# Performance work log

Hardware: AMD Instinct MI355X
Metric: run time of the kernel (lower is better)

## Reference

```python
import jax, jax.numpy as jnp
import numpy as np

B, S, D, H = 2, 2048, 1024, 16
DK = D // H
NEG = -65504.0  # matches torch masked_fill value in source


def setup_inputs() -> dict:
    key = jax.random.key(0)
    ks = jax.random.split(key, 5)
    scale = 1.0 / np.sqrt(D)
    return {
        "x": jax.random.normal(ks[0], (B, S, D), dtype=jnp.float32),
        "W_q": jax.random.normal(ks[1], (D, D), dtype=jnp.float32) * scale,
        "W_k": jax.random.normal(ks[2], (D, D), dtype=jnp.float32) * scale,
        "W_v": jax.random.normal(ks[3], (D, D), dtype=jnp.float32) * scale,
        "W_o": jax.random.normal(ks[4], (D, D), dtype=jnp.float32) * scale,
    }


def reference(x, W_q, W_k, W_v, W_o):
    b, s, d = x.shape
    # nn.Linear(x) = x @ W.T ; split heads -> [b, h, s, dk]
    def proj(W):
        return (x @ W.T).reshape(b, s, H, DK).transpose(0, 2, 1, 3)
    q, k, v = proj(W_q), proj(W_k), proj(W_v)
    scores = jnp.einsum("bhqd,bhkd->bhqk", q, k) / jnp.sqrt(jnp.float32(DK))
    causal = jnp.tril(jnp.ones((s, s), dtype=bool))  # True where attending allowed
    scores = jnp.where(causal, scores, NEG)
    attn = jax.nn.softmax(scores, axis=-1)  # attn_pdrop=0 -> dropout is identity
    out = jnp.einsum("bhqk,bhkd->bhqd", attn, v)
    out = out.transpose(0, 2, 1, 3).reshape(b, s, d)
    return out @ W_o.T
```

## Files before the change

kernel.cpp:

```cpp
#include <hip/hip_runtime.h>
#include <hip/hip_bf16.h>

typedef __attribute__((ext_vector_type(4))) float f32x4;
typedef __attribute__((ext_vector_type(8))) short bf16x8;

#define Bn 2
#define Sn 2048
#define Dn 1024
#define Hn 16
#define DKn 64
#define Mrows (Bn * Sn)

__device__ __forceinline__ unsigned short f2bf(float f) {
  unsigned int x = __float_as_uint(f);
  x += 0x7fffu + ((x >> 16) & 1u);
  return (unsigned short)(x >> 16);
}

__device__ __forceinline__ float bf2f(unsigned short u) {
  return __uint_as_float(((unsigned int)u) << 16);
}

__device__ __forceinline__ unsigned int cvtpk(float lo, float hi) {
  unsigned int r;
  asm("v_cvt_pk_bf16_f32 %0, %1, %2" : "=v"(r) : "v"(lo), "v"(hi));
  return r;
}

__device__ __forceinline__ float exp2a(float x) {
  float r;
  asm("v_exp_f32 %0, %1" : "=v"(r) : "v"(x));
  return r;
}

__device__ __forceinline__ f32x4 mfma16(bf16x8 a, bf16x8 b, f32x4 c) {
  return __builtin_amdgcn_mfma_f32_16x16x32_bf16(a, b, c, 0, 0, 0);
}

__device__ __forceinline__ f32x4 max4(f32x4 a, f32x4 b) {
  f32x4 r;
  r[0] = fmaxf(a[0], b[0]); r[1] = fmaxf(a[1], b[1]);
  r[2] = fmaxf(a[2], b[2]); r[3] = fmaxf(a[3], b[3]);
  return r;
}

__device__ __forceinline__ void gload_lds16(const unsigned short* g, unsigned short* l) {
  __builtin_amdgcn_global_load_lds(
      (const __attribute__((address_space(1))) void*)g,
      (__attribute__((address_space(3))) void*)l, 16, 0, 0);
}

__global__ __launch_bounds__(256)
void cvt_all(const float* __restrict__ x,  const float* __restrict__ wq,
             const float* __restrict__ wk, const float* __restrict__ wv,
             const float* __restrict__ wo,
             unsigned short* __restrict__ xb,  unsigned short* __restrict__ wqb,
             unsigned short* __restrict__ wkb, unsigned short* __restrict__ wvb,
             unsigned short* __restrict__ wob) {
  int i = (blockIdx.x * 256 + threadIdx.x) * 4;
  const float* src; unsigned short* dst; int off;
  int r = i >> 20;
  if (r < 4)       { src = x;  dst = xb;  off = i; }
  else if (r == 4) { src = wq; dst = wqb; off = i & 1048575; }
  else if (r == 5) { src = wk; dst = wkb; off = i & 1048575; }
  else if (r == 6) { src = wv; dst = wvb; off = i & 1048575; }
  else             { src = wo; dst = wob; off = i & 1048575; }
  float4 v = *(const float4*)(src + off);
  ushort4 o;
  o.x = f2bf(v.x); o.y = f2bf(v.y); o.z = f2bf(v.z); o.w = f2bf(v.w);
  *(ushort4*)(dst + off) = o;
}

template<int MODE>
__device__ __forceinline__ void gemm_body(const unsigned short* __restrict__ A,
                                          const unsigned short* __restrict__ W,
                                          unsigned short* __restrict__ Cb,
                                          float* __restrict__ Cf,
                                          unsigned short* As,
                                          unsigned short* Bs,
                                          int row0, int col0) {
  const int K = Dn, N = Dn;
  const int tid  = threadIdx.x;
  const int wid  = tid >> 6;
  const int lane = tid & 63;
  const int l15  = lane & 15;
  const int lg   = lane >> 4;
  const int wr = (wid >> 1) * 64;
  const int wc = (wid & 1) * 64;

  f32x4 acc[4][4] = {};

  const int lrow2 = lane >> 2;
  const int gs    = (lane & 3) ^ ((lane >> 3) & 3);
  const int swzr  = (l15 >> 1) & 3;

  auto stage = [&](int kt, int b) {
#pragma unroll
    for (int q = 0; q < 2; ++q) {
      int chunk = wid * 2 + q;
      int r = chunk * 16 + lrow2;
      gload_lds16(A + (size_t)(row0 + r) * K + kt + gs * 8,
                  &As[b * 4096 + chunk * 512]);
    }
#pragma unroll
    for (int q = 0; q < 2; ++q) {
      int chunk = wid * 2 + q;
      int r = chunk * 16 + lrow2;
      gload_lds16(W + (size_t)(col0 + r) * K + kt + gs * 8,
                  &Bs[b * 4096 + chunk * 512]);
    }
  };

  auto compute = [&](int b) {
    bf16x8 af[4], bfr[4];
#pragma unroll
    for (int m = 0; m < 4; ++m)
      af[m] = *(const bf16x8*)(&As[b * 4096 + (wr + m * 16 + l15) * 32 +
                                   ((lg ^ swzr) * 8)]);
#pragma unroll
    for (int n = 0; n < 4; ++n)
      bfr[n] = *(const bf16x8*)(&Bs[b * 4096 + (wc + n * 16 + l15) * 32 +
                                    ((lg ^ swzr) * 8)]);
    __builtin_amdgcn_s_setprio(1);
#pragma unroll
    for (int m = 0; m < 4; ++m)
#pragma unroll
      for (int n = 0; n < 4; ++n)
        acc[m][n] = mfma16(af[m], bfr[n], acc[m][n]);
    __builtin_amdgcn_s_setprio(0);
  };

  stage(0, 0);
  stage(32, 1);
  int cb = 0;
#pragma unroll 1
  for (int t = 0; t < 32; ++t) {
    if (t < 31) asm volatile("s_waitcnt vmcnt(4)" ::: "memory");
    else        asm volatile("s_waitcnt vmcnt(0)" ::: "memory");
    __builtin_amdgcn_sched_barrier(0);
    __builtin_amdgcn_s_barrier();
    __builtin_amdgcn_sched_barrier(0);
    if (t <= 29) {
      int sb = cb + 2; if (sb >= 3) sb -= 3;
      stage((t + 2) * 32, sb);
    }
    compute(cb);
    ++cb; if (cb == 3) cb = 0;
  }

#pragma unroll
  for (int m = 0; m < 4; ++m)
#pragma unroll
    for (int n = 0; n < 4; ++n) {
      int r0 = row0 + wr + m * 16 + lg * 4;
      int c  = col0 + wc + n * 16 + l15;
      if (MODE == 2) {
        int b = r0 >> 11, s = r0 & 2047;
        int h = c >> 6,  d = c & 63;
        ushort4 pw;
        pw.x = f2bf(acc[m][n][0]); pw.y = f2bf(acc[m][n][1]);
        pw.z = f2bf(acc[m][n][2]); pw.w = f2bf(acc[m][n][3]);
        *(ushort4*)(Cb + ((((size_t)b * Hn + h) * DKn + d) << 11) + s) = pw;
      } else {
#pragma unroll
        for (int j = 0; j < 4; ++j) {
          size_t idx = (size_t)(r0 + j) * N + c;
          float v = acc[m][n][j];
          if (MODE == 3)      Cf[idx] = v;
          else if (MODE == 0) Cb[idx] = f2bf(v * 0.18033688f);
          else                Cb[idx] = f2bf(v);
        }
      }
    }
}

__global__ __launch_bounds__(256, 3)
void gemm_qkv(const unsigned short* __restrict__ A,
              const unsigned short* __restrict__ W0,
              const unsigned short* __restrict__ W1,
              const unsigned short* __restrict__ W2,
              unsigned short* __restrict__ C0,
              unsigned short* __restrict__ C1,
              unsigned short* __restrict__ C2) {
  __shared__ unsigned short As[3 * 128 * 32];
  __shared__ unsigned short Bs[3 * 128 * 32];
  const int fid = blockIdx.x;
  const int panel = fid % 24;
  const int row0 = (fid / 24) * 128;
  const int col0 = (panel & 7) * 128;
  const int z = panel >> 3;
  if (z == 0)      gemm_body<0>(A, W0, C0, nullptr, As, Bs, row0, col0);
  else if (z == 1) gemm_body<1>(A, W1, C1, nullptr, As, Bs, row0, col0);
  else             gemm_body<2>(A, W2, C2, nullptr, As, Bs, row0, col0);
}

__global__ __launch_bounds__(256, 3)
void gemm_out(const unsigned short* __restrict__ A,
              const unsigned short* __restrict__ W,
              float* __restrict__ C) {
  __shared__ unsigned short As[3 * 128 * 32];
  __shared__ unsigned short Bs[3 * 128 * 32];
  gemm_body<3>(A, W, nullptr, C, As, Bs, blockIdx.x * 128, blockIdx.y * 128);
}

__global__ __launch_bounds__(256, 3)
void attn_part(const unsigned short* __restrict__ Qg,
               const unsigned short* __restrict__ Kg,
               const unsigned short* __restrict__ Vtg,
               unsigned short* __restrict__ Og,
               unsigned short* __restrict__ Pb,
               float* __restrict__ Pml) {
  const int bid = blockIdx.x;
  const int bh = bid & 31;
  const int j  = bid >> 5;
  const int bb = bh >> 4, hh = bh & 15;
  const int tid = threadIdx.x, wid = tid >> 6, lane = tid & 63;
  const int l15 = lane & 15, lg = lane >> 4;
  const int wq = wid * 32;
  const size_t baseQ = (size_t)bb * Sn * Dn + (size_t)hh * DKn;
  const size_t baseV = (size_t)bh * DKn * Sn;

  __shared__ unsigned short Ks[2][64 * 64];
  __shared__ unsigned short Vts[2][64 * 64];
  __shared__ unsigned short Ps[4][32 * 72];

  const int lrow  = lane >> 3;
  const int sgran = (lane & 7) ^ lrow;
  const int swz   = l15 & 7;

  const int bstart = (34 * j) / 3;
  const int nt = (34 * (j + 1)) / 3 - bstart;

  int qt = 0;
  while ((qt + 1) * (qt + 2) <= bstart) ++qt;
  int kt = bstart - qt * (qt + 1);

  int sqt = qt, skt = kt;
  auto stage = [&](int t, int b) {
    const int k0 = t << 6;
#pragma unroll
    for (int p = 0; p < 2; ++p) {
      int c = p * 4 + wid;
      int r = c * 8 + lrow;
      gload_lds16(Kg + baseQ + (size_t)(k0 + r) * Dn + sgran * 8, &Ks[b][c * 512]);
    }
#pragma unroll
    for (int p = 0; p < 2; ++p) {
      int c = p * 4 + wid;
      int dr = c * 8 + lrow;
      gload_lds16(Vtg + baseV + (size_t)dr * Sn + k0 + sgran * 8, &Vts[b][c * 512]);
    }
  };
  auto advs = [&]() { ++skt; if (skt == 2 * sqt + 2) { skt = 0; ++sqt; } };

  stage(skt, 0); advs();
  __syncthreads();

  bf16x8 qf[2][2];
  auto loadQ = [&](int qtile) {
    const int q0 = qtile * 128;
#pragma unroll
    for (int qm = 0; qm < 2; ++qm)
#pragma unroll
      for (int kd = 0; kd < 2; ++kd)
        qf[qm][kd] = *(const bf16x8*)(Qg + baseQ +
                     (size_t)(q0 + wq + qm * 16 + l15) * Dn + kd * 32 + lg * 8);
  };
  loadQ(qt);

  f32x4 oacc[2][4] = {};
  float mrun[2] = {-1e30f, -1e30f};
  float lrun[2] = {0.f, 0.f};
  int pstart = kt;

  for (int i = 0; i < nt; ++i) {
    const int cur = i & 1;
    if (i < nt - 1) { stage(skt, cur ^ 1); advs(); }
    const int k0 = kt << 6;
    const int q0 = qt * 128;

    if (k0 <= q0 + wq + 31) {
      f32x4 sf[2][4] = {};
      __builtin_amdgcn_s_setprio(1);
#pragma unroll
      for (int kn = 0; kn < 4; ++kn)
#pragma unroll
        for (int kd = 0; kd < 2; ++kd) {
          bf16x8 kf = *(const bf16x8*)(&Ks[cur][(kn * 16 + l15) * 64 +
                                              (((kd * 4 + lg) ^ swz) * 8)]);
          sf[0][kn] = mfma16(kf, qf[0][kd], sf[0][kn]);
          sf[1][kn] = mfma16(kf, qf[1][kd], sf[1][kn]);
        }
      __builtin_amdgcn_s_setprio(0);

      if (k0 + 63 > q0 + wq) {
#pragma unroll
        for (int qm = 0; qm < 2; ++qm) {
          int qq = q0 + wq + qm * 16 + l15;
#pragma unroll
          for (int kn = 0; kn < 4; ++kn)
#pragma unroll
            for (int jj = 0; jj < 4; ++jj) {
              int key = k0 + kn * 16 + lg * 4 + jj;
              if (key > qq) sf[qm][kn][jj] = -1e30f;
            }
        }
      }

#pragma unroll
      for (int qm = 0; qm < 2; ++qm) {
        f32x4 mm = max4(max4(sf[qm][0], sf[qm][1]), max4(sf[qm][2], sf[qm][3]));
        float tl = fmaxf(fmaxf(mm[0], mm[1]), fmaxf(mm[2], mm[3]));
        if (__any(tl > mrun[qm] + 11.5f)) {
          float t = tl;
          t = fmaxf(t, __shfl_xor(t, 16));
          t = fmaxf(t, __shfl_xor(t, 32));
          float mnew = fmaxf(mrun[qm], t);
          float corr = exp2a(mrun[qm] - mnew);
          mrun[qm] = mnew;
          lrun[qm] *= corr;
#pragma unroll
          for (int dn = 0; dn < 4; ++dn) oacc[qm][dn] *= corr;
        }
        const float m = mrun[qm];
#pragma unroll
        for (int kn = 0; kn < 4; ++kn) {
#pragma unroll
          for (int jj = 0; jj < 4; ++jj)
            sf[qm][kn][jj] = exp2a(sf[qm][kn][jj] - m);
          uint2 pw;
          pw.x = cvtpk(sf[qm][kn][0], sf[qm][kn][1]);
          pw.y = cvtpk(sf[qm][kn][2], sf[qm][kn][3]);
          *(uint2*)(&Ps[wid][(qm * 16 + l15) * 72 + kn * 16 + lg * 4]) = pw;
        }
        f32x4 sv = (sf[qm][0] + sf[qm][1]) + (sf[qm][2] + sf[qm][3]);
        lrun[qm] += (sv[0] + sv[1]) + (sv[2] + sv[3]);
      }

      __builtin_amdgcn_s_setprio(1);
#pragma unroll
      for (int kk = 0; kk < 2; ++kk) {
        bf16x8 pf[2];
#pragma unroll
        for (int qm = 0; qm < 2; ++qm)
          pf[qm] = *(const bf16x8*)(&Ps[wid][(qm * 16 + l15) * 72 + kk * 32 + lg * 8]);
#pragma unroll
        for (int dn = 0; dn < 4; ++dn) {
          bf16x8 vf = *(const bf16x8*)(&Vts[cur][(dn * 16 + l15) * 64 +
                                               (((kk * 4 + lg) ^ swz) * 8)]);
#pragma unroll
          for (int qm = 0; qm < 2; ++qm)
            oacc[qm][dn] = mfma16(vf, pf[qm], oacc[qm][dn]);
        }
      }
      __builtin_amdgcn_s_setprio(0);
    }

    const bool segend = (kt == 2 * qt + 1);
    if (segend || i == nt - 1) {
      if (pstart == 0 && segend) {
#pragma unroll
        for (int qm = 0; qm < 2; ++qm) {
          float lt = lrun[qm];
          lt += __shfl_xor(lt, 16);
          lt += __shfl_xor(lt, 32);
          float rinv = 1.0f / lt;
          int row = q0 + wq + qm * 16 + l15;
#pragma unroll
          for (int dn = 0; dn < 4; ++dn) {
            ushort4 ow;
            ow.x = f2bf(oacc[qm][dn][0] * rinv);
            ow.y = f2bf(oacc[qm][dn][1] * rinv);
            ow.z = f2bf(oacc[qm][dn][2] * rinv);
            ow.w = f2bf(oacc[qm][dn][3] * rinv);
            *(ushort4*)(Og + baseQ + (size_t)row * Dn + dn * 16 + lg * 4) = ow;
          }
        }
      } else {
        const size_t slot = (size_t)bh * 40 + (pstart == 0 ? qt : 16 + j);
#pragma unroll
        for (int qm = 0; qm < 2; ++qm) {
          float lt = lrun[qm];
          lt += __shfl_xor(lt, 16);
          lt += __shfl_xor(lt, 32);
          int rl = wq + qm * 16 + l15;
#pragma unroll
          for (int dn = 0; dn < 4; ++dn) {
            ushort4 ow;
            ow.x = f2bf(oacc[qm][dn][0]);
            ow.y = f2bf(oacc[qm][dn][1]);
            ow.z = f2bf(oacc[qm][dn][2]);
            ow.w = f2bf(oacc[qm][dn][3]);
            *(ushort4*)(Pb + slot * 8192 + (size_t)rl * 64 + dn * 16 + lg * 4) = ow;
          }
          if (lg == 0) {
            Pml[slot * 256 + rl] = mrun[qm];
            Pml[slot * 256 + 128 + rl] = lt;
          }
        }
      }
      if (i < nt - 1) {
        ++qt; kt = 0; pstart = 0;
        loadQ(qt);
#pragma unroll
        for (int qm = 0; qm < 2; ++qm) {
          mrun[qm] = -1e30f; lrun[qm] = 0.f;
#pragma unroll
          for (int dn = 0; dn < 4; ++dn) oacc[qm][dn] = f32x4{0.f, 0.f, 0.f, 0.f};
        }
      }
    } else {
      ++kt;
    }
    __syncthreads();
  }
}

__global__ __launch_bounds__(256)
void attn_combine(const unsigned short* __restrict__ Pb,
                  const float* __restrict__ Pml,
                  unsigned short* __restrict__ Og) {
  const int b = blockIdx.x;
  const int bh = b >> 4, qt = b & 15;
  const int s = qt * (qt + 1);
  const int e = s + 2 * qt + 2;
  const int js = (3 * s + 2) / 34;
  const int je = (3 * (e - 1) + 2) / 34;
  const int np = je - js + 1;
  if (np == 1) return;
  const int bb = bh >> 4, hh = bh & 15;
  const size_t baseQ = (size_t)bb * Sn * Dn + (size_t)hh * DKn;
  const int q0 = qt * 128;
  const int r = threadIdx.x >> 1;
  const int c32 = (threadIdx.x & 1) * 32;

  float M = -1e30f;
  for (int p = 0; p < np; ++p) {
    size_t slot = (size_t)bh * 40 + (p == 0 ? qt : 16 + js + p);
    M = fmaxf(M, Pml[slot * 256 + r]);
  }

  float L = 0.f;
  float acc[32];
#pragma unroll
  for (int k = 0; k < 32; ++k) acc[k] = 0.f;
  for (int p = 0; p < np; ++p) {
    size_t slot = (size_t)bh * 40 + (p == 0 ? qt : 16 + js + p);
    float w = exp2a(Pml[slot * 256 + r] - M);
    L += Pml[slot * 256 + 128 + r] * w;
    const unsigned short* src = Pb + slot * 8192 + (size_t)r * 64 + c32;
#pragma unroll
    for (int k4 = 0; k4 < 8; ++k4) {
      ushort4 v = *(const ushort4*)(src + k4 * 4);
      acc[k4 * 4 + 0] += w * bf2f(v.x);
      acc[k4 * 4 + 1] += w * bf2f(v.y);
      acc[k4 * 4 + 2] += w * bf2f(v.z);
      acc[k4 * 4 + 3] += w * bf2f(v.w);
    }
  }

  float rinv = 1.0f / L;
#pragma unroll
  for (int k4 = 0; k4 < 8; ++k4) {
    ushort4 o;
    o.x = f2bf(acc[k4 * 4 + 0] * rinv);
    o.y = f2bf(acc[k4 * 4 + 1] * rinv);
    o.z = f2bf(acc[k4 * 4 + 2] * rinv);
    o.w = f2bf(acc[k4 * 4 + 3] * rinv);
    *(ushort4*)(Og + baseQ + (size_t)(q0 + r) * Dn + c32 + k4 * 4) = o;
  }
}

extern "C" void kernel_launch(void* const* d_in, const int* in_sizes, int n_in,
                              void* d_out, int out_size, void* d_ws, size_t ws_size,
                              hipStream_t stream) {
  const float* x  = (const float*)d_in[0];
  const float* Wq = (const float*)d_in[1];
  const float* Wk = (const float*)d_in[2];
  const float* Wv = (const float*)d_in[3];
  const float* Wo = (const float*)d_in[4];
  float* out = (float*)d_out;

  char* ws = (char*)d_ws;
  size_t off = 0;
  unsigned short* xb  = (unsigned short*)(ws + off); off += (size_t)Mrows * Dn * 2;
  unsigned short* wqb = (unsigned short*)(ws + off); off += (size_t)Dn * Dn * 2;
  unsigned short* wkb = (unsigned short*)(ws + off); off += (size_t)Dn * Dn * 2;
  unsigned short* wvb = (unsigned short*)(ws + off); off += (size_t)Dn * Dn * 2;
  unsigned short* wob = (unsigned short*)(ws + off); off += (size_t)Dn * Dn * 2;
  unsigned short* Qb  = (unsigned short*)(ws + off); off += (size_t)Mrows * Dn * 2;
  unsigned short* Kb  = (unsigned short*)(ws + off); off += (size_t)Mrows * Dn * 2;
  unsigned short* Vtb = (unsigned short*)(ws + off); off += (size_t)Mrows * Dn * 2;
  unsigned short* Ob  = (unsigned short*)(ws + off); off += (size_t)Mrows * Dn * 2;
  unsigned short* Pb  = (unsigned short*)(ws + off); off += (size_t)1280 * 8192 * 2;
  float*          Pml = (float*)(ws + off);          off += (size_t)1280 * 256 * 4;

  cvt_all<<<8192, 256, 0, stream>>>(x, Wq, Wk, Wv, Wo, xb, wqb, wkb, wvb, wob);
  gemm_qkv<<<768, 256, 0, stream>>>(xb, wqb, wkb, wvb, Qb, Kb, Vtb);
  attn_part<<<768, 256, 0, stream>>>(Qb, Kb, Vtb, Ob, Pb, Pml);
  attn_combine<<<512, 256, 0, stream>>>(Pb, Pml, Ob);
  gemm_out<<<dim3(Mrows / 128, Dn / 128), 256, 0, stream>>>(Ob, wob, out);
}
```

Measured before the change: 110.2 us.

## Use 8-wave attention blocks with 16-row warps and uniform 17-tile work split

The attention partial kernel now runs 512 threads (8 waves), each wave owning 16 query rows instead of 32, which halves per-wave register state and allows more resident waves. Work is split evenly into 512 blocks of exactly 17 key tiles each, and partial-result slots are re-indexed per query tile (up to 3 per tile), with the combine kernel rewritten to use this fixed layout. This aims to improve latency hiding and load balance, at the cost of less reuse of each K/V fragment across query rows and more LDS reads per MFMA.

```diff
diff --git a/kernel.cpp b/kernel.cpp
--- a/kernel.cpp
+++ b/kernel.cpp
@@ -203,7 +203,7 @@
   gemm_body<3>(A, W, nullptr, C, As, Bs, blockIdx.x * 128, blockIdx.y * 128);
 }
 
-__global__ __launch_bounds__(256, 3)
+__global__ __launch_bounds__(512, 4)
 void attn_part(const unsigned short* __restrict__ Qg,
                const unsigned short* __restrict__ Kg,
                const unsigned short* __restrict__ Vtg,
@@ -216,71 +216,59 @@
   const int bb = bh >> 4, hh = bh & 15;
   const int tid = threadIdx.x, wid = tid >> 6, lane = tid & 63;
   const int l15 = lane & 15, lg = lane >> 4;
-  const int wq = wid * 32;
+  const int wq = wid * 16;
   const size_t baseQ = (size_t)bb * Sn * Dn + (size_t)hh * DKn;
   const size_t baseV = (size_t)bh * DKn * Sn;
 
   __shared__ unsigned short Ks[2][64 * 64];
   __shared__ unsigned short Vts[2][64 * 64];
-  __shared__ unsigned short Ps[4][32 * 72];
+  __shared__ unsigned short Ps[8][16 * 72];
 
   const int lrow  = lane >> 3;
   const int sgran = (lane & 7) ^ lrow;
   const int swz   = l15 & 7;
 
-  const int bstart = (34 * j) / 3;
-  const int nt = (34 * (j + 1)) / 3 - bstart;
-
+  const int g0 = 17 * j;
   int qt = 0;
-  while ((qt + 1) * (qt + 2) <= bstart) ++qt;
-  int kt = bstart - qt * (qt + 1);
+  while ((qt + 1) * (qt + 2) <= g0) ++qt;
+  int kt = g0 - qt * (qt + 1);
 
   int sqt = qt, skt = kt;
   auto stage = [&](int t, int b) {
     const int k0 = t << 6;
-#pragma unroll
-    for (int p = 0; p < 2; ++p) {
-      int c = p * 4 + wid;
-      int r = c * 8 + lrow;
-      gload_lds16(Kg + baseQ + (size_t)(k0 + r) * Dn + sgran * 8, &Ks[b][c * 512]);
-    }
-#pragma unroll
-    for (int p = 0; p < 2; ++p) {
-      int c = p * 4 + wid;
-      int dr = c * 8 + lrow;
-      gload_lds16(Vtg + baseV + (size_t)dr * Sn + k0 + sgran * 8, &Vts[b][c * 512]);
-    }
+    gload_lds16(Kg + baseQ + (size_t)(k0 + wid * 8 + lrow) * Dn + sgran * 8,
+                &Ks[b][wid * 512]);
+    gload_lds16(Vtg + baseV + (size_t)(wid * 8 + lrow) * Sn + k0 + sgran * 8,
+                &Vts[b][wid * 512]);
   };
   auto advs = [&]() { ++skt; if (skt == 2 * sqt + 2) { skt = 0; ++sqt; } };
 
   stage(skt, 0); advs();
   __syncthreads();
 
-  bf16x8 qf[2][2];
+  bf16x8 qf[2];
   auto loadQ = [&](int qtile) {
     const int q0 = qtile * 128;
 #pragma unroll
-    for (int qm = 0; qm < 2; ++qm)
-#pragma unroll
-      for (int kd = 0; kd < 2; ++kd)
-        qf[qm][kd] = *(const bf16x8*)(Qg + baseQ +
-                     (size_t)(q0 + wq + qm * 16 + l15) * Dn + kd * 32 + lg * 8);
+    for (int kd = 0; kd < 2; ++kd)
+      qf[kd] = *(const bf16x8*)(Qg + baseQ +
+               (size_t)(q0 + wq + l15) * Dn + kd * 32 + lg * 8);
   };
   loadQ(qt);
 
-  f32x4 oacc[2][4] = {};
-  float mrun[2] = {-1e30f, -1e30f};
-  float lrun[2] = {0.f, 0.f};
+  f32x4 oacc[4] = {};
+  float mrun = -1e30f;
+  float lrun = 0.f;
   int pstart = kt;
 
-  for (int i = 0; i < nt; ++i) {
+  for (int i = 0; i < 17; ++i) {
     const int cur = i & 1;
-    if (i < nt - 1) { stage(skt, cur ^ 1); advs(); }
+    if (i < 16) { stage(skt, cur ^ 1); advs(); }
     const int k0 = kt << 6;
     const int q0 = qt * 128;
 
-    if (k0 <= q0 + wq + 31) {
-      f32x4 sf[2][4] = {};
+    if (k0 <= q0 + wq + 15) {
+      f32x4 sf[4] = {};
       __builtin_amdgcn_s_setprio(1);
 #pragma unroll
       for (int kn = 0; kn < 4; ++kn)
@@ -288,126 +276,107 @@
         for (int kd = 0; kd < 2; ++kd) {
           bf16x8 kf = *(const bf16x8*)(&Ks[cur][(kn * 16 + l15) * 64 +
                                               (((kd * 4 + lg) ^ swz) * 8)]);
-          sf[0][kn] = mfma16(kf, qf[0][kd], sf[0][kn]);
-          sf[1][kn] = mfma16(kf, qf[1][kd], sf[1][kn]);
+          sf[kn] = mfma16(kf, qf[kd], sf[kn]);
         }
       __builtin_amdgcn_s_setprio(0);
 
       if (k0 + 63 > q0 + wq) {
-#pragma unroll
-        for (int qm = 0; qm < 2; ++qm) {
-          int qq = q0 + wq + qm * 16 + l15;
-#pragma unroll
-          for (int kn = 0; kn < 4; ++kn)
-#pragma unroll
-            for (int jj = 0; jj < 4; ++jj) {
-              int key = k0 + kn * 16 + lg * 4 + jj;
-              if (key > qq) sf[qm][kn][jj] = -1e30f;
-            }
-        }
-      }
-
-#pragma unroll
-      for (int qm = 0; qm < 2; ++qm) {
-        f32x4 mm = max4(max4(sf[qm][0], sf[qm][1]), max4(sf[qm][2], sf[qm][3]));
-        float tl = fmaxf(fmaxf(mm[0], mm[1]), fmaxf(mm[2], mm[3]));
-        if (__any(tl > mrun[qm] + 11.5f)) {
-          float t = tl;
-          t = fmaxf(t, __shfl_xor(t, 16));
-          t = fmaxf(t, __shfl_xor(t, 32));
-          float mnew = fmaxf(mrun[qm], t);
-          float corr = exp2a(mrun[qm] - mnew);
-          mrun[qm] = mnew;
-          lrun[qm] *= corr;
-#pragma unroll
-          for (int dn = 0; dn < 4; ++dn) oacc[qm][dn] *= corr;
-        }
-        const float m = mrun[qm];
-#pragma unroll
-        for (int kn = 0; kn < 4; ++kn) {
-#pragma unroll
-          for (int jj = 0; jj < 4; ++jj)
-            sf[qm][kn][jj] = exp2a(sf[qm][kn][jj] - m);
-          uint2 pw;
-          pw.x = cvtpk(sf[qm][kn][0], sf[qm][kn][1]);
-          pw.y = cvtpk(sf[qm][kn][2], sf[qm][kn][3]);
-          *(uint2*)(&Ps[wid][(qm * 16 + l15) * 72 + kn * 16 + lg * 4]) = pw;
-        }
-        f32x4 sv = (sf[qm][0] + sf[qm][1]) + (sf[qm][2] + sf[qm][3]);
-        lrun[qm] += (sv[0] + sv[1]) + (sv[2] + sv[3]);
-      }
+        int qq = q0 + wq + l15;
+#pragma unroll
+        for (int kn = 0; kn < 4; ++kn)
+#pragma unroll
+          for (int jj = 0; jj < 4; ++jj) {
+            int key = k0 + kn * 16 + lg * 4 + jj;
+            if (key > qq) sf[kn][jj] = -1e30f;
+          }
+      }
+
+      f32x4 mm = max4(max4(sf[0], sf[1]), max4(sf[2], sf[3]));
+      float tl = fmaxf(fmaxf(mm[0], mm[1]), fmaxf(mm[2], mm[3]));
+      if (__any(tl > mrun + 11.5f)) {
+        float t = tl;
+        t = fmaxf(t, __shfl_xor(t, 16));
+        t = fmaxf(t, __shfl_xor(t, 32));
+        float mnew = fmaxf(mrun, t);
+        float corr = exp2a(mrun - mnew);
+        mrun = mnew;
+        lrun *= corr;
+#pragma unroll
+        for (int dn = 0; dn < 4; ++dn) oacc[dn] *= corr;
+      }
+      const float m = mrun;
+#pragma unroll
+      for (int kn = 0; kn < 4; ++kn) {
+#pragma unroll
+        for (int jj = 0; jj < 4; ++jj)
+          sf[kn][jj] = exp2a(sf[kn][jj] - m);
+        uint2 pw;
+        pw.x = cvtpk(sf[kn][0], sf[kn][1]);
+        pw.y = cvtpk(sf[kn][2], sf[kn][3]);
+        *(uint2*)(&Ps[wid][l15 * 72 + kn * 16 + lg * 4]) = pw;
+      }
+      f32x4 sv = (sf[0] + sf[1]) + (sf[2] + sf[3]);
+      lrun += (sv[0] + sv[1]) + (sv[2] + sv[3]);
 
       __builtin_amdgcn_s_setprio(1);
 #pragma unroll
       for (int kk = 0; kk < 2; ++kk) {
-        bf16x8 pf[2];
-#pragma unroll
-        for (int qm = 0; qm < 2; ++qm)
-          pf[qm] = *(const bf16x8*)(&Ps[wid][(qm * 16 + l15) * 72 + kk * 32 + lg * 8]);
+        bf16x8 pf = *(const bf16x8*)(&Ps[wid][l15 * 72 + kk * 32 + lg * 8]);
 #pragma unroll
         for (int dn = 0; dn < 4; ++dn) {
           bf16x8 vf = *(const bf16x8*)(&Vts[cur][(dn * 16 + l15) * 64 +
                                                (((kk * 4 + lg) ^ swz) * 8)]);
-#pragma unroll
-          for (int qm = 0; qm < 2; ++qm)
-            oacc[qm][dn] = mfma16(vf, pf[qm], oacc[qm][dn]);
+          oacc[dn] = mfma16(vf, pf, oacc[dn]);
         }
       }
       __builtin_amdgcn_s_setprio(0);
     }
 
     const bool segend = (kt == 2 * qt + 1);
-    if (segend || i == nt - 1) {
+    if (segend || i == 16) {
       if (pstart == 0 && segend) {
-#pragma unroll
-        for (int qm = 0; qm < 2; ++qm) {
-          float lt = lrun[qm];
-          lt += __shfl_xor(lt, 16);
-          lt += __shfl_xor(lt, 32);
-          float rinv = 1.0f / lt;
-          int row = q0 + wq + qm * 16 + l15;
-#pragma unroll
-          for (int dn = 0; dn < 4; ++dn) {
-            ushort4 ow;
-            ow.x = f2bf(oacc[qm][dn][0] * rinv);
-            ow.y = f2bf(oacc[qm][dn][1] * rinv);
-            ow.z = f2bf(oacc[qm][dn][2] * rinv);
-            ow.w = f2bf(oacc[qm][dn][3] * rinv);
-            *(ushort4*)(Og + baseQ + (size_t)row * Dn + dn * 16 + lg * 4) = ow;
-          }
+        float lt = lrun;
+        lt += __shfl_xor(lt, 16);
+        lt += __shfl_xor(lt, 32);
+        float rinv = 1.0f / lt;
+        int row = q0 + wq + l15;
+#pragma unroll
+        for (int dn = 0; dn < 4; ++dn) {
+          ushort4 ow;
+          ow.x = f2bf(oacc[dn][0] * rinv);
+          ow.y = f2bf(oacc[dn][1] * rinv);
+          ow.z = f2bf(oacc[dn][2] * rinv);
+          ow.w = f2bf(oacc[dn][3] * rinv);
+          *(ushort4*)(Og + baseQ + (size_t)row * Dn + dn * 16 + lg * 4) = ow;
         }
       } else {
-        const size_t slot = (size_t)bh * 40 + (pstart == 0 ? qt : 16 + j);
-#pragma unroll
-        for (int qm = 0; qm < 2; ++qm) {
-          float lt = lrun[qm];
-          lt += __shfl_xor(lt, 16);
-          lt += __shfl_xor(lt, 32);
-          int rl = wq + qm * 16 + l15;
-#pragma unroll
-          for (int dn = 0; dn < 4; ++dn) {
-            ushort4 ow;
-            ow.x = f2bf(oacc[qm][dn][0]);
-            ow.y = f2bf(oacc[qm][dn][1]);
-            ow.z = f2bf(oacc[qm][dn][2]);
-            ow.w = f2bf(oacc[qm][dn][3]);
-            *(ushort4*)(Pb + slot * 8192 + (size_t)rl * 64 + dn * 16 + lg * 4) = ow;
-          }
-          if (lg == 0) {
-            Pml[slot * 256 + rl] = mrun[qm];
-            Pml[slot * 256 + 128 + rl] = lt;
-          }
-        }
-      }
-      if (i < nt - 1) {
+        const int seg_s = qt * (qt + 1);
+        const int ord = pstart ? ((seg_s + pstart) / 17 - seg_s / 17) : 0;
+        const size_t slot = (size_t)((bh * 16 + qt) * 3 + ord);
+        float lt = lrun;
+        lt += __shfl_xor(lt, 16);
+        lt += __shfl_xor(lt, 32);
+        int rl = wq + l15;
+#pragma unroll
+        for (int dn = 0; dn < 4; ++dn) {
+          ushort4 ow;
+          ow.x = f2bf(oacc[dn][0]);
+          ow.y = f2bf(oacc[dn][1]);
+          ow.z = f2bf(oacc[dn][2]);
+          ow.w = f2bf(oacc[dn][3]);
+          *(ushort4*)(Pb + slot * 8192 + (size_t)rl * 64 + dn * 16 + lg * 4) = ow;
+        }
+        if (lg == 0) {
+          Pml[slot * 256 + rl] = mrun;
+          Pml[slot * 256 + 128 + rl] = lt;
+        }
+      }
+      if (i < 16) {
         ++qt; kt = 0; pstart = 0;
         loadQ(qt);
-#pragma unroll
-        for (int qm = 0; qm < 2; ++qm) {
-          mrun[qm] = -1e30f; lrun[qm] = 0.f;
-#pragma unroll
-          for (int dn = 0; dn < 4; ++dn) oacc[qm][dn] = f32x4{0.f, 0.f, 0.f, 0.f};
-        }
+        mrun = -1e30f; lrun = 0.f;
+#pragma unroll
+        for (int dn = 0; dn < 4; ++dn) oacc[dn] = f32x4{0.f, 0.f, 0.f, 0.f};
       }
     } else {
       ++kt;
@@ -422,33 +391,38 @@
                   unsigned short* __restrict__ Og) {
   const int b = blockIdx.x;
   const int bh = b >> 4, qt = b & 15;
-  const int s = qt * (qt + 1);
-  const int e = s + 2 * qt + 2;
-  const int js = (3 * s + 2) / 34;
-  const int je = (3 * (e - 1) + 2) / 34;
-  const int np = je - js + 1;
-  if (np == 1) return;
+  const int seg_s = qt * (qt + 1);
+  const int seg_e = seg_s + 2 * qt + 2;
+  const int c0 = (seg_s / 17 + 1) * 17;
+  if (c0 >= seg_e) return;
+  const int np = (c0 + 17 < seg_e) ? 3 : 2;
   const int bb = bh >> 4, hh = bh & 15;
   const size_t baseQ = (size_t)bb * Sn * Dn + (size_t)hh * DKn;
   const int q0 = qt * 128;
+  const int slot0 = b * 3;
   const int r = threadIdx.x >> 1;
   const int c32 = (threadIdx.x & 1) * 32;
 
-  float M = -1e30f;
-  for (int p = 0; p < np; ++p) {
-    size_t slot = (size_t)bh * 40 + (p == 0 ? qt : 16 + js + p);
-    M = fmaxf(M, Pml[slot * 256 + r]);
+  float m0 = Pml[(size_t)slot0 * 256 + r];
+  float l0 = Pml[(size_t)slot0 * 256 + 128 + r];
+  float m1 = Pml[(size_t)(slot0 + 1) * 256 + r];
+  float l1 = Pml[(size_t)(slot0 + 1) * 256 + 128 + r];
+  float m2 = -1e30f, l2 = 0.f;
+  if (np == 3) {
+    m2 = Pml[(size_t)(slot0 + 2) * 256 + r];
+    l2 = Pml[(size_t)(slot0 + 2) * 256 + 128 + r];
   }
-
-  float L = 0.f;
+  float M = fmaxf(fmaxf(m0, m1), m2);
+  float w0 = exp2a(m0 - M), w1 = exp2a(m1 - M);
+  float w2 = (np == 3) ? exp2a(m2 - M) : 0.f;
+  float L = l0 * w0 + l1 * w1 + l2 * w2;
+
   float acc[32];
 #pragma unroll
   for (int k = 0; k < 32; ++k) acc[k] = 0.f;
-  for (int p = 0; p < np; ++p) {
-    size_t slot = (size_t)bh * 40 + (p == 0 ? qt : 16 + js + p);
-    float w = exp2a(Pml[slot * 256 + r] - M);
-    L += Pml[slot * 256 + 128 + r] * w;
-    const unsigned short* src = Pb + slot * 8192 + (size_t)r * 64 + c32;
+
+  auto accum = [&](int p, float w) {
+    const unsigned short* src = Pb + (size_t)(slot0 + p) * 8192 + (size_t)r * 64 + c32;
 #pragma unroll
     for (int k4 = 0; k4 < 8; ++k4) {
       ushort4 v = *(const ushort4*)(src + k4 * 4);
@@ -457,7 +431,10 @@
       acc[k4 * 4 + 2] += w * bf2f(v.z);
       acc[k4 * 4 + 3] += w * bf2f(v.w);
     }
-  }
+  };
+  accum(0, w0);
+  accum(1, w1);
+  if (np == 3) accum(2, w2);
 
   float rinv = 1.0f / L;
 #pragma unroll
@@ -492,12 +469,12 @@
   unsigned short* Kb  = (unsigned short*)(ws + off); off += (size_t)Mrows * Dn * 2;
   unsigned short* Vtb = (unsigned short*)(ws + off); off += (size_t)Mrows * Dn * 2;
   unsigned short* Ob  = (unsigned short*)(ws + off); off += (size_t)Mrows * Dn * 2;
-  unsigned short* Pb  = (unsigned short*)(ws + off); off += (size_t)1280 * 8192 * 2;
-  float*          Pml = (float*)(ws + off);          off += (size_t)1280 * 256 * 4;
+  unsigned short* Pb  = (unsigned short*)(ws + off); off += (size_t)1536 * 8192 * 2;
+  float*          Pml = (float*)(ws + off);          off += (size_t)1536 * 256 * 4;
 
   cvt_all<<<8192, 256, 0, stream>>>(x, Wq, Wk, Wv, Wo, xb, wqb, wkb, wvb, wob);
   gemm_qkv<<<768, 256, 0, stream>>>(xb, wqb, wkb, wvb, Qb, Kb, Vtb);
-  attn_part<<<768, 256, 0, stream>>>(Qb, Kb, Vtb, Ob, Pb, Pml);
+  attn_part<<<512, 512, 0, stream>>>(Qb, Kb, Vtb, Ob, Pb, Pml);
   attn_combine<<<512, 256, 0, stream>>>(Pb, Pml, Ob);
   gemm_out<<<dim3(Mrows / 128, Dn / 128), 256, 0, stream>>>(Ob, wob, out);
 }
```

After: 109.8 us. Within noise of the previous version (-0.4%).

## Enlarge attention Q tile to 256 rows with 512-thread blocks

Applied to the files above, without the earlier changes.

Doubles the attention query tile from 128 to 256 rows by using 8 waves per block, so each K/V tile staged in LDS is reused by twice as many query rows. The work split becomes a fixed 9 key tiles per block over 512 blocks, and the partial-result slots and combine kernel are resized to match. The larger tile halves K/V global traffic per query, but it gives fewer blocks, more threads per block, and a different load balance across the causal triangle.

```diff
diff --git a/kernel.cpp b/kernel.cpp
--- a/kernel.cpp
+++ b/kernel.cpp
@@ -203,7 +203,7 @@
   gemm_body<3>(A, W, nullptr, C, As, Bs, blockIdx.x * 128, blockIdx.y * 128);
 }
 
-__global__ __launch_bounds__(256, 3)
+__global__ __launch_bounds__(512, 4)
 void attn_part(const unsigned short* __restrict__ Qg,
                const unsigned short* __restrict__ Kg,
                const unsigned short* __restrict__ Vtg,
@@ -222,43 +222,33 @@
 
   __shared__ unsigned short Ks[2][64 * 64];
   __shared__ unsigned short Vts[2][64 * 64];
-  __shared__ unsigned short Ps[4][32 * 72];
+  __shared__ unsigned short Ps[8][32 * 72];
 
   const int lrow  = lane >> 3;
   const int sgran = (lane & 7) ^ lrow;
   const int swz   = l15 & 7;
 
-  const int bstart = (34 * j) / 3;
-  const int nt = (34 * (j + 1)) / 3 - bstart;
-
+  const int g0 = 9 * j;
   int qt = 0;
-  while ((qt + 1) * (qt + 2) <= bstart) ++qt;
-  int kt = bstart - qt * (qt + 1);
+  while (2 * (qt + 1) * (qt + 2) <= g0) ++qt;
+  int kt = g0 - 2 * qt * (qt + 1);
 
   int sqt = qt, skt = kt;
   auto stage = [&](int t, int b) {
     const int k0 = t << 6;
-#pragma unroll
-    for (int p = 0; p < 2; ++p) {
-      int c = p * 4 + wid;
-      int r = c * 8 + lrow;
-      gload_lds16(Kg + baseQ + (size_t)(k0 + r) * Dn + sgran * 8, &Ks[b][c * 512]);
-    }
-#pragma unroll
-    for (int p = 0; p < 2; ++p) {
-      int c = p * 4 + wid;
-      int dr = c * 8 + lrow;
-      gload_lds16(Vtg + baseV + (size_t)dr * Sn + k0 + sgran * 8, &Vts[b][c * 512]);
-    }
+    gload_lds16(Kg + baseQ + (size_t)(k0 + wid * 8 + lrow) * Dn + sgran * 8,
+                &Ks[b][wid * 512]);
+    gload_lds16(Vtg + baseV + (size_t)(wid * 8 + lrow) * Sn + k0 + sgran * 8,
+                &Vts[b][wid * 512]);
   };
-  auto advs = [&]() { ++skt; if (skt == 2 * sqt + 2) { skt = 0; ++sqt; } };
+  auto advs = [&]() { ++skt; if (skt == 4 * sqt + 4) { skt = 0; ++sqt; } };
 
   stage(skt, 0); advs();
   __syncthreads();
 
   bf16x8 qf[2][2];
   auto loadQ = [&](int qtile) {
-    const int q0 = qtile * 128;
+    const int q0 = qtile * 256;
 #pragma unroll
     for (int qm = 0; qm < 2; ++qm)
 #pragma unroll
@@ -273,11 +263,11 @@
   float lrun[2] = {0.f, 0.f};
   int pstart = kt;
 
-  for (int i = 0; i < nt; ++i) {
+  for (int i = 0; i < 9; ++i) {
     const int cur = i & 1;
-    if (i < nt - 1) { stage(skt, cur ^ 1); advs(); }
+    if (i < 8) { stage(skt, cur ^ 1); advs(); }
     const int k0 = kt << 6;
-    const int q0 = qt * 128;
+    const int q0 = qt << 8;
 
     if (k0 <= q0 + wq + 31) {
       f32x4 sf[2][4] = {};
@@ -356,8 +346,8 @@
       __builtin_amdgcn_s_setprio(0);
     }
 
-    const bool segend = (kt == 2 * qt + 1);
-    if (segend || i == nt - 1) {
+    const bool segend = (kt == 4 * qt + 3);
+    if (segend || i == 8) {
       if (pstart == 0 && segend) {
 #pragma unroll
         for (int qm = 0; qm < 2; ++qm) {
@@ -377,7 +367,7 @@
           }
         }
       } else {
-        const size_t slot = (size_t)bh * 40 + (pstart == 0 ? qt : 16 + j);
+        const size_t slot = (size_t)bh * 24 + (pstart == 0 ? qt : 8 + j);
 #pragma unroll
         for (int qm = 0; qm < 2; ++qm) {
           float lt = lrun[qm];
@@ -391,15 +381,15 @@
             ow.y = f2bf(oacc[qm][dn][1]);
             ow.z = f2bf(oacc[qm][dn][2]);
             ow.w = f2bf(oacc[qm][dn][3]);
-            *(ushort4*)(Pb + slot * 8192 + (size_t)rl * 64 + dn * 16 + lg * 4) = ow;
+            *(ushort4*)(Pb + slot * 16384 + (size_t)rl * 64 + dn * 16 + lg * 4) = ow;
           }
           if (lg == 0) {
-            Pml[slot * 256 + rl] = mrun[qm];
-            Pml[slot * 256 + 128 + rl] = lt;
+            Pml[slot * 512 + rl] = mrun[qm];
+            Pml[slot * 512 + 256 + rl] = lt;
           }
         }
       }
-      if (i < nt - 1) {
+      if (i < 8) {
         ++qt; kt = 0; pstart = 0;
         loadQ(qt);
 #pragma unroll
@@ -416,28 +406,28 @@
   }
 }
 
-__global__ __launch_bounds__(256)
+__global__ __launch_bounds__(512)
 void attn_combine(const unsigned short* __restrict__ Pb,
                   const float* __restrict__ Pml,
                   unsigned short* __restrict__ Og) {
-  const int b = blockIdx.x;
-  const int bh = b >> 4, qt = b & 15;
-  const int s = qt * (qt + 1);
-  const int e = s + 2 * qt + 2;
-  const int js = (3 * s + 2) / 34;
-  const int je = (3 * (e - 1) + 2) / 34;
+  const int bid = blockIdx.x;
+  const int qt = bid >> 5, bh = bid & 31;
+  const int seg_s = 2 * qt * (qt + 1);
+  const int seg_e = 2 * (qt + 1) * (qt + 2);
+  const int js = seg_s / 9;
+  const int je = (seg_e - 1) / 9;
   const int np = je - js + 1;
   if (np == 1) return;
   const int bb = bh >> 4, hh = bh & 15;
   const size_t baseQ = (size_t)bb * Sn * Dn + (size_t)hh * DKn;
-  const int q0 = qt * 128;
+  const int q0 = qt * 256;
   const int r = threadIdx.x >> 1;
   const int c32 = (threadIdx.x & 1) * 32;
 
   float M = -1e30f;
   for (int p = 0; p < np; ++p) {
-    size_t slot = (size_t)bh * 40 + (p == 0 ? qt : 16 + js + p);
-    M = fmaxf(M, Pml[slot * 256 + r]);
+    size_t slot = (size_t)bh * 24 + (p == 0 ? qt : 8 + js + p);
+    M = fmaxf(M, Pml[slot * 512 + r]);
   }
 
   float L = 0.f;
@@ -445,10 +435,10 @@
 #pragma unroll
   for (int k = 0; k < 32; ++k) acc[k] = 0.f;
   for (int p = 0; p < np; ++p) {
-    size_t slot = (size_t)bh * 40 + (p == 0 ? qt : 16 + js + p);
-    float w = exp2a(Pml[slot * 256 + r] - M);
-    L += Pml[slot * 256 + 128 + r] * w;
-    const unsigned short* src = Pb + slot * 8192 + (size_t)r * 64 + c32;
+    size_t slot = (size_t)bh * 24 + (p == 0 ? qt : 8 + js + p);
+    float w = exp2a(Pml[slot * 512 + r] - M);
+    L += Pml[slot * 512 + 256 + r] * w;
+    const unsigned short* src = Pb + slot * 16384 + (size_t)r * 64 + c32;
 #pragma unroll
     for (int k4 = 0; k4 < 8; ++k4) {
       ushort4 v = *(const ushort4*)(src + k4 * 4);
@@ -492,12 +482,12 @@
   unsigned short* Kb  = (unsigned short*)(ws + off); off += (size_t)Mrows * Dn * 2;
   unsigned short* Vtb = (unsigned short*)(ws + off); off += (size_t)Mrows * Dn * 2;
   unsigned short* Ob  = (unsigned short*)(ws + off); off += (size_t)Mrows * Dn * 2;
-  unsigned short* Pb  = (unsigned short*)(ws + off); off += (size_t)1280 * 8192 * 2;
-  float*          Pml = (float*)(ws + off);          off += (size_t)1280 * 256 * 4;
+  unsigned short* Pb  = (unsigned short*)(ws + off); off += (size_t)32 * 24 * 16384 * 2;
+  float*          Pml = (float*)(ws + off);          off += (size_t)32 * 24 * 512 * 4;
 
   cvt_all<<<8192, 256, 0, stream>>>(x, Wq, Wk, Wv, Wo, xb, wqb, wkb, wvb, wob);
   gemm_qkv<<<768, 256, 0, stream>>>(xb, wqb, wkb, wvb, Qb, Kb, Vtb);
-  attn_part<<<768, 256, 0, stream>>>(Qb, Kb, Vtb, Ob, Pb, Pml);
-  attn_combine<<<512, 256, 0, stream>>>(Pb, Pml, Ob);
+  attn_part<<<512, 512, 0, stream>>>(Qb, Kb, Vtb, Ob, Pb, Pml);
+  attn_combine<<<256, 512, 0, stream>>>(Pb, Pml, Ob);
   gemm_out<<<dim3(Mrows / 128, Dn / 128), 256, 0, stream>>>(Ob, wob, out);
 }
```

Result: no change. 110.6 us (+0.3%).
